# Performance work log

Measured on AMD Instinct MI355X. Metric: run time of the kernel, lower is better.

## Reference

```python
import jax, jax.numpy as jnp
import numpy as np
from jax import lax

B, N, SEG, T = 64, 19, 15, 400
FIN, HID, K, NH, DM, FF, L, NC = 64, 128, 4, 4, 64, 128, 4, 3
EPS = 1e-5


def setup_inputs() -> dict:
    key = jax.random.key(0)
    ks = jax.random.split(key, 40)
    nrm = lambda i, s, sc=0.05: jax.random.normal(ks[i], s, dtype=jnp.float32) * sc
    inp = {
        "X": jax.random.normal(ks[0], (B, N, SEG, T), dtype=jnp.float32),
        "A_hat": jax.random.uniform(ks[1], (B, K, SEG, N, N), dtype=jnp.float32),
        "conv1_w": nrm(2, (32, 1, 25)), "conv1_b": nrm(3, (32,)),
        "conv2_w": nrm(4, (64, 32, 9)), "conv2_b": nrm(5, (64,)),
        "g1_W": nrm(6, (HID, FIN)), "g1_q": nrm(7, (K,), 1.0),
        "g1_bn_g": jnp.ones((HID,)), "g1_bn_b": jnp.zeros((HID,)),
        "g1_bn_m": jnp.zeros((HID,)), "g1_bn_v": jnp.ones((HID,)),
        "g2_W": nrm(8, (FIN, HID)), "g2_q": nrm(9, (K,), 1.0),
        "g2_bn_g": jnp.ones((FIN,)), "g2_bn_b": jnp.zeros((FIN,)),
        "g2_bn_m": jnp.zeros((FIN,)), "g2_bn_v": jnp.ones((FIN,)),
        "cls_token": nrm(10, (1, 1, DM), 0.02), "pos_emb": nrm(11, (1, SEG + 1, DM), 0.02),
        "t_wqkv": nrm(12, (L, 3 * DM, DM)), "t_bqkv": nrm(13, (L, 3 * DM)),
        "t_wo": nrm(14, (L, DM, DM)), "t_bo": nrm(15, (L, DM)),
        "t_ln1g": jnp.ones((L, DM)), "t_ln1b": jnp.zeros((L, DM)),
        "t_w1": nrm(16, (L, FF, DM)), "t_b1": nrm(17, (L, FF)),
        "t_w2": nrm(18, (L, DM, FF)), "t_b2": nrm(19, (L, DM)),
        "t_ln2g": jnp.ones((L, DM)), "t_ln2b": jnp.zeros((L, DM)),
        "clf_w": nrm(20, (NC, DM)), "clf_b": nrm(21, (NC,)),
    }
    return inp


def _ln(x, g, b):
    mu = x.mean(-1, keepdims=True)
    v = ((x - mu) ** 2).mean(-1, keepdims=True)
    return (x - mu) * lax.rsqrt(v + EPS) * g + b


def _maxpool(x, w):  # x: [M, C, T]
    return lax.reduce_window(x, -jnp.inf, lax.max, (1, 1, w), (1, 1, w), "VALID")


def _temporal_encoder(X, c1w, c1b, c2w, c2b):
    # X: [B, SEG, N, T] -> [B, SEG, N, FIN]
    x = X.reshape(-1, 1, T)
    dn = ("NCH", "OIH", "NCH")
    x = lax.conv_general_dilated(x, c1w, (4,), [(12, 12)], dimension_numbers=dn) + c1b[None, :, None]
    x = _maxpool(jax.nn.relu(x), 4)                      # [M,32,25]
    x = lax.conv_general_dilated(x, c2w, (2,), [(4, 4)], dimension_numbers=dn) + c2b[None, :, None]
    x = _maxpool(jax.nn.relu(x), 2)                      # [M,64,6]
    x = x.mean(-1)                                       # AdaptiveAvgPool1d(1)
    return x.reshape(B, SEG, N, FIN)


def _gcn(Xf, A, W, q, g, b, m, v):
    alpha = jax.nn.softmax(q)                            # [K]
    AX = jnp.einsum("bksnm,bsmf->bksnf", A, Xf)          # K-hop diffusion
    Hk = jnp.einsum("bksnf,of->bksno", AX, W)            # shared linear
    H = jnp.einsum("k,bksno->bsno", alpha, Hk)           # attn-weighted hop mix
    H = (H - m) * lax.rsqrt(v + EPS) * g + b             # eval-mode BatchNorm1d
    return jax.nn.relu(H)


def _forward(X, A_hat, conv1_w, conv1_b, conv2_w, conv2_b,
             g1_W, g1_q, g1_bn_g, g1_bn_b, g1_bn_m, g1_bn_v,
             g2_W, g2_q, g2_bn_g, g2_bn_b, g2_bn_m, g2_bn_v,
             cls_token, pos_emb, t_wqkv, t_bqkv, t_wo, t_bo,
             t_ln1g, t_ln1b, t_w1, t_b1, t_w2, t_b2, t_ln2g, t_ln2b,
             clf_w, clf_b):
    Xs = X.reshape(-1, N, SEG, T).transpose(0, 2, 1, 3)  # [B,SEG,N,T]
    feat = _temporal_encoder(Xs, conv1_w, conv1_b, conv2_w, conv2_b)
    H = _gcn(feat, A_hat, g1_W, g1_q, g1_bn_g, g1_bn_b, g1_bn_m, g1_bn_v)
    H = _gcn(H, A_hat, g2_W, g2_q, g2_bn_g, g2_bn_b, g2_bn_m, g2_bn_v)
    g = H.mean(axis=2)                                   # node-mean -> [B,SEG,DM]
    x = jnp.concatenate([jnp.broadcast_to(cls_token, (B, 1, DM)), g], axis=1)
    x = x + pos_emb[:, : SEG + 1]
    dh = DM // NH
    for l in range(L):
        qkv = x @ t_wqkv[l].T + t_bqkv[l]
        qh, kh, vh = [u.reshape(B, SEG + 1, NH, dh).transpose(0, 2, 1, 3)
                      for u in jnp.split(qkv, 3, axis=-1)]
        attn = jax.nn.softmax(jnp.einsum("bhqd,bhkd->bhqk", qh, kh) / jnp.sqrt(jnp.float32(dh)), axis=-1)
        o = jnp.einsum("bhqk,bhkd->bhqd", attn, vh).transpose(0, 2, 1, 3).reshape(B, SEG + 1, DM)
        x = _ln(x + o @ t_wo[l].T + t_bo[l], t_ln1g[l], t_ln1b[l])
        ff = jax.nn.relu(x @ t_w1[l].T + t_b1[l]) @ t_w2[l].T + t_b2[l]
        x = _ln(x + ff, t_ln2g[l], t_ln2b[l])
    return x[:, 0] @ clf_w.T + clf_b                     # [B, NC]


def reference(X, A_hat, conv1_w, conv1_b, conv2_w, conv2_b,
              g1_W, g1_q, g1_bn_g, g1_bn_b, g1_bn_m, g1_bn_v,
              g2_W, g2_q, g2_bn_g, g2_bn_b, g2_bn_m, g2_bn_v,
              cls_token, pos_emb, t_wqkv, t_bqkv, t_wo, t_bo,
              t_ln1g, t_ln1b, t_w1, t_b1, t_w2, t_b2, t_ln2g, t_ln2b,
              clf_w, clf_b):
    return _forward(X, A_hat, conv1_w, conv1_b, conv2_w, conv2_b,
                    g1_W, g1_q, g1_bn_g, g1_bn_b, g1_bn_m, g1_bn_v,
                    g2_W, g2_q, g2_bn_g, g2_bn_b, g2_bn_m, g2_bn_v,
                    cls_token, pos_emb, t_wqkv, t_bqkv, t_wo, t_bo,
                    t_ln1g, t_ln1b, t_w1, t_b1, t_w2, t_b2, t_ln2g, t_ln2b,
                    clf_w, clf_b)
```

## Files before the change

### kernel.cpp

```cpp
#include <hip/hip_runtime.h>
#include <cmath>

#define B_ 64
#define N_ 19
#define SEG_ 15
#define T_ 400
#define FIN_ 64
#define HID_ 128
#define K_ 4
#define NH_ 4
#define DM_ 64
#define FF_ 128
#define L_ 4
#define NC_ 3
#define EPS_ 1e-5f

typedef __attribute__((ext_vector_type(8))) short bf16x8;
typedef __attribute__((ext_vector_type(4))) float f32x4;
typedef unsigned short ushort_t;

__device__ __forceinline__ ushort_t f2bf(float x) {
  union { float f; unsigned u; } a; a.f = x;
  unsigned r = a.u + 0x7fffu + ((a.u >> 16) & 1u);
  return (ushort_t)(r >> 16);
}
__device__ __forceinline__ float bf2f(ushort_t h) {
  union { unsigned u; float f; } a; a.u = ((unsigned)h) << 16;
  return a.f;
}

__global__ __launch_bounds__(256) void k_prep(
    const float* __restrict__ c2w,
    const float* __restrict__ wqkv, const float* __restrict__ wo,
    const float* __restrict__ w1, const float* __restrict__ w2,
    const float* __restrict__ g1W, const float* __restrict__ g2W,
    ushort_t* __restrict__ bt,
    ushort_t* __restrict__ Th, ushort_t* __restrict__ Tl,
    ushort_t* __restrict__ W1h, ushort_t* __restrict__ W1l,
    ushort_t* __restrict__ W2h, ushort_t* __restrict__ W2l) {
  int gid = blockIdx.x * 256 + threadIdx.x;
  if (gid < 18944) {
    int oc = gid / 296, k = gid - oc * 296;
    int ic = k & 31, kk = k >> 5;
    ushort_t v = 0;
    if (kk < 9) v = f2bf(c2w[oc * 288 + ic * 9 + kk]);
    bt[gid] = v;
  } else if (gid < 68096) {
    int i = gid - 18944;
    int l = i / 12288, r = i % 12288;
    float v = wqkv[i];
    ushort_t h = f2bf(v);
    int dst = l * 32768 + r;
    Th[dst] = h; Tl[dst] = f2bf(v - bf2f(h));
  } else if (gid < 84480) {
    int i = gid - 68096;
    int l = i / 4096, r = i % 4096;
    float v = wo[i];
    ushort_t h = f2bf(v);
    int dst = l * 32768 + 12288 + r;
    Th[dst] = h; Tl[dst] = f2bf(v - bf2f(h));
  } else if (gid < 117248) {
    int i = gid - 84480;
    int l = i / 8192, r = i % 8192;
    float v = w1[i];
    ushort_t h = f2bf(v);
    int dst = l * 32768 + 16384 + r;
    Th[dst] = h; Tl[dst] = f2bf(v - bf2f(h));
  } else if (gid < 150016) {
    int i = gid - 117248;
    int l = i / 8192, r = i % 8192;
    float v = w2[i];
    ushort_t h = f2bf(v);
    int dst = l * 32768 + 24576 + r;
    Th[dst] = h; Tl[dst] = f2bf(v - bf2f(h));
  } else if (gid < 158208) {
    int i = gid - 150016;
    float v = g1W[i];
    ushort_t h = f2bf(v);
    W1h[i] = h;
    W1l[i] = f2bf(v - bf2f(h));
  } else if (gid < 166400) {
    int i = gid - 158208;
    float v = g2W[i];
    ushort_t h = f2bf(v);
    W2h[i] = h;
    W2l[i] = f2bf(v - bf2f(h));
  }
}

#define RPB 4
#define ICP 40
#define P1R 40
#define OFFB_XP 0
#define OFFB_W1 6784
#define OFFB_P1 9984
#define SMEM_T 22784

__global__ __launch_bounds__(256, 4) void k_temporal(
    const float* __restrict__ X, const float* __restrict__ c1w,
    const float* __restrict__ c1b, const float* __restrict__ c2b,
    const ushort_t* __restrict__ BmatT, float* __restrict__ Xf) {
  __shared__ __align__(16) unsigned char smem[SMEM_T];
  float* xp  = (float*)(smem + OFFB_XP);
  float* w1s = (float*)(smem + OFFB_W1);
  ushort_t* p1T = (ushort_t*)(smem + OFFB_P1);
  float* Dbuf = (float*)(smem + OFFB_XP);

  const int tid = threadIdx.x;
  const int row0 = blockIdx.x * RPB;

  for (int i = tid; i < 800; i += 256) w1s[i] = c1w[i];
  for (int i = tid; i < RPB * P1R * ICP / 2; i += 256) ((unsigned*)p1T)[i] = 0u;
  for (int r = 0; r < RPB; ++r) {
    const int gr = row0 + r;
    const int n = gr % N_;
    const int s = (gr / N_) % SEG_;
    const int b = gr / (N_ * SEG_);
    const float* xin = X + (((size_t)b * N_ + n) * SEG_ + s) * T_;
    for (int i = tid; i < 424; i += 256) {
      int t = i - 12;
      xp[r * 424 + i] = (t >= 0 && t < T_) ? xin[t] : 0.f;
    }
  }
  __syncthreads();

  {
    const int oc = tid & 31, sub = tid >> 5;
    float wr[25];
#pragma unroll
    for (int k = 0; k < 25; ++k) wr[k] = w1s[oc * 25 + k];
    const float bias = c1b[oc];
    for (int r = 0; r < RPB; ++r) {
      const float* xb = xp + r * 424;
      for (int j = sub; j < 25; j += 8) {
        float xr[37];
#pragma unroll
        for (int k = 0; k < 37; ++k) xr[k] = xb[16 * j + k];
        float m = -1e30f;
#pragma unroll
        for (int p = 0; p < 4; ++p) {
          float acc = bias;
#pragma unroll
          for (int k = 0; k < 25; ++k) acc += xr[4 * p + k] * wr[k];
          m = fmaxf(m, acc);
        }
        p1T[(r * P1R + j + 4) * ICP + oc] = f2bf(fmaxf(m, 0.f));
      }
    }
  }
  __syncthreads();

  const int lane = tid & 63, wv = tid >> 6;
  const int quad = lane >> 4, nl = lane & 15;
  f32x4 acc[4];
  int abase[4];
#pragma unroll
  for (int tm = 0; tm < 4; ++tm) {
    acc[tm] = (f32x4){0.f, 0.f, 0.f, 0.f};
    int m = tm * 16 + nl;
    int rl = m / 14;
    int op = m - rl * 14;
    if (rl > 3) rl = 3;
    if (op > 13) op = 13;
    abase[tm] = (rl * P1R + 2 * op) * ICP + quad * 8;
  }
  const ushort_t* brow = BmatT + (wv * 16 + nl) * 296 + quad * 8;
#pragma unroll
  for (int kk = 0; kk < 9; ++kk) {
    bf16x8 bfr = *(const bf16x8*)(brow + kk * 32);
#pragma unroll
    for (int tm = 0; tm < 4; ++tm) {
      bf16x8 afr = *(const bf16x8*)(p1T + abase[tm] + kk * ICP);
      acc[tm] = __builtin_amdgcn_mfma_f32_16x16x32_bf16(afr, bfr, acc[tm], 0, 0, 0);
    }
  }
  __syncthreads();

#pragma unroll
  for (int tm = 0; tm < 4; ++tm)
#pragma unroll
    for (int rg = 0; rg < 4; ++rg)
      Dbuf[(tm * 16 + quad * 4 + rg) * 66 + wv * 16 + nl] = acc[tm][rg];
  __syncthreads();

  for (int o = tid; o < RPB * 64; o += 256) {
    int rl = o >> 6, oc = o & 63;
    float bias = c2b[oc];
    const float* dr = Dbuf + (rl * 14) * 66 + oc;
    float s = 0.f;
#pragma unroll
    for (int jj = 0; jj < 6; ++jj) {
      float v = fmaxf(dr[(2 * jj) * 66], dr[(2 * jj + 1) * 66]) + bias;
      s += fmaxf(v, 0.f);
    }
    Xf[(size_t)(row0 + rl) * FIN_ + oc] = s * (1.f / 6.f);
  }
}

__global__ __launch_bounds__(256) void k_gcn(
    const float* __restrict__ A, const float* __restrict__ Xf,
    const ushort_t* __restrict__ W1h, const ushort_t* __restrict__ W1l,
    const ushort_t* __restrict__ W2h, const ushort_t* __restrict__ W2l,
    const float* __restrict__ q1, const float* __restrict__ q2,
    const float* __restrict__ b1g, const float* __restrict__ b1b,
    const float* __restrict__ b1m, const float* __restrict__ b1v,
    const float* __restrict__ b2g, const float* __restrict__ b2b,
    const float* __restrict__ b2m, const float* __restrict__ b2v,
    float* __restrict__ G) {
  const int bs = blockIdx.x;
  const int b = bs / SEG_;
  const int s = bs % SEG_;
  const int tid = threadIdx.x;

  __shared__ __align__(16) ushort_t xh[32 * 72], xl[32 * 72];
  __shared__ __align__(16) ushort_t Hh[32 * 136], Hl[32 * 136];
  __shared__ float abar1[N_ * N_], abar2[N_ * N_];
  __shared__ float ybuf[N_ * 130];
  __shared__ float zbuf[N_ * 64];
  __shared__ float sc1[HID_], sh1[HID_], sc2[FIN_], sh2[FIN_];

  {
    float p0 = q1[0], p1 = q1[1], p2 = q1[2], p3 = q1[3];
    float mx = fmaxf(fmaxf(p0, p1), fmaxf(p2, p3));
    float e0 = expf(p0 - mx), e1 = expf(p1 - mx), e2 = expf(p2 - mx), e3 = expf(p3 - mx);
    float inv = 1.f / (e0 + e1 + e2 + e3);
    float a0 = e0 * inv, a1 = e1 * inv, a2 = e2 * inv, a3 = e3 * inv;
    float r0 = q2[0], r1 = q2[1], r2 = q2[2], r3 = q2[3];
    float mx2 = fmaxf(fmaxf(r0, r1), fmaxf(r2, r3));
    float f0 = expf(r0 - mx2), f1 = expf(r1 - mx2), f2 = expf(r2 - mx2), f3 = expf(r3 - mx2);
    float inv2 = 1.f / (f0 + f1 + f2 + f3);
    float c0 = f0 * inv2, c1 = f1 * inv2, c2 = f2 * inv2, c3 = f3 * inv2;
    const size_t kstride = (size_t)SEG_ * N_ * N_;
    const float* Ab = A + ((size_t)b * K_ * SEG_ + s) * (N_ * N_);
    for (int i = tid; i < N_ * N_; i += 256) {
      float v0 = Ab[i], v1 = Ab[i + kstride], v2 = Ab[i + 2 * kstride], v3 = Ab[i + 3 * kstride];
      abar1[i] = a0 * v0 + a1 * v1 + a2 * v2 + a3 * v3;
      abar2[i] = c0 * v0 + c1 * v1 + c2 * v2 + c3 * v3;
    }
  }

  for (int i = tid; i < 32 * 72 / 2; i += 256) {
    ((unsigned*)xh)[i] = 0u; ((unsigned*)xl)[i] = 0u;
  }
  for (int i = tid; i < 32 * 136 / 2; i += 256) {
    ((unsigned*)Hh)[i] = 0u; ((unsigned*)Hl)[i] = 0u;
  }
  for (int o = tid; o < HID_; o += 256) {
    float sc = b1g[o] * rsqrtf(b1v[o] + EPS_);
    sc1[o] = sc; sh1[o] = b1b[o] - b1m[o] * sc;
  }
  for (int o = tid; o < FIN_; o += 256) {
    float sc = b2g[o] * rsqrtf(b2v[o] + EPS_);
    sc2[o] = sc; sh2[o] = b2b[o] - b2m[o] * sc;
  }
  __syncthreads();

  const float* xb = Xf + (size_t)bs * N_ * FIN_;
  for (int i = tid; i < N_ * FIN_; i += 256) {
    int r = i >> 6, f = i & 63;
    float v = xb[i];
    ushort_t h = f2bf(v);
    xh[r * 72 + f] = h;
    xl[r * 72 + f] = f2bf(v - bf2f(h));
  }
  __syncthreads();

  const int lane = tid & 63, wv = tid >> 6;
  const int quad = lane >> 4, nl = lane & 15;

#pragma unroll
  for (int mt = 0; mt < 2; ++mt) {
#pragma unroll
    for (int ntl = 0; ntl < 2; ++ntl) {
      const int nt = wv * 2 + ntl;
      f32x4 acc = (f32x4){0.f, 0.f, 0.f, 0.f};
#pragma unroll
      for (int ks = 0; ks < 2; ++ks) {
        bf16x8 ah = *(const bf16x8*)(xh + (mt * 16 + nl) * 72 + ks * 32 + quad * 8);
        bf16x8 al = *(const bf16x8*)(xl + (mt * 16 + nl) * 72 + ks * 32 + quad * 8);
        bf16x8 bh = *(const bf16x8*)(W1h + (nt * 16 + nl) * 64 + ks * 32 + quad * 8);
        bf16x8 bl = *(const bf16x8*)(W1l + (nt * 16 + nl) * 64 + ks * 32 + quad * 8);
        acc = __builtin_amdgcn_mfma_f32_16x16x32_bf16(ah, bh, acc, 0, 0, 0);
        acc = __builtin_amdgcn_mfma_f32_16x16x32_bf16(al, bh, acc, 0, 0, 0);
        acc = __builtin_amdgcn_mfma_f32_16x16x32_bf16(ah, bl, acc, 0, 0, 0);
      }
#pragma unroll
      for (int r = 0; r < 4; ++r) {
        int m = mt * 16 + quad * 4 + r;
        if (m < N_) ybuf[m * 130 + nt * 16 + nl] = acc[r];
      }
    }
  }
  __syncthreads();

  for (int idx = tid; idx < N_ * HID_; idx += 256) {
    int nn = idx >> 7, o = idx & 127;
    float acc = 0.f;
    const float* ar = &abar1[nn * N_];
#pragma unroll
    for (int m = 0; m < N_; ++m) acc += ar[m] * ybuf[m * 130 + o];
    float h = fmaxf(acc * sc1[o] + sh1[o], 0.f);
    ushort_t hh = f2bf(h);
    Hh[nn * 136 + o] = hh;
    Hl[nn * 136 + o] = f2bf(h - bf2f(hh));
  }
  __syncthreads();

  {
    const int nt = wv;
#pragma unroll
    for (int mt = 0; mt < 2; ++mt) {
      f32x4 acc = (f32x4){0.f, 0.f, 0.f, 0.f};
#pragma unroll
      for (int ks = 0; ks < 4; ++ks) {
        bf16x8 ah = *(const bf16x8*)(Hh + (mt * 16 + nl) * 136 + ks * 32 + quad * 8);
        bf16x8 al = *(const bf16x8*)(Hl + (mt * 16 + nl) * 136 + ks * 32 + quad * 8);
        bf16x8 bh = *(const bf16x8*)(W2h + (nt * 16 + nl) * 128 + ks * 32 + quad * 8);
        bf16x8 bl = *(const bf16x8*)(W2l + (nt * 16 + nl) * 128 + ks * 32 + quad * 8);
        acc = __builtin_amdgcn_mfma_f32_16x16x32_bf16(ah, bh, acc, 0, 0, 0);
        acc = __builtin_amdgcn_mfma_f32_16x16x32_bf16(al, bh, acc, 0, 0, 0);
        acc = __builtin_amdgcn_mfma_f32_16x16x32_bf16(ah, bl, acc, 0, 0, 0);
      }
#pragma unroll
      for (int r = 0; r < 4; ++r) {
        int m = mt * 16 + quad * 4 + r;
        if (m < N_) ybuf[m * 66 + nt * 16 + nl] = acc[r];
      }
    }
  }
  __syncthreads();

  for (int idx = tid; idx < N_ * FIN_; idx += 256) {
    int nn = idx >> 6, o = idx & 63;
    float acc = 0.f;
    const float* ar = &abar2[nn * N_];
#pragma unroll
    for (int m = 0; m < N_; ++m) acc += ar[m] * ybuf[m * 66 + o];
    zbuf[idx] = fmaxf(acc * sc2[o] + sh2[o], 0.f);
  }
  __syncthreads();

  if (tid < FIN_) {
    float ssum = 0.f;
#pragma unroll
    for (int nn = 0; nn < N_; ++nn) ssum += zbuf[nn * 64 + tid];
    G[(size_t)bs * FIN_ + tid] = ssum * (1.f / (float)N_);
  }
}

__global__ __launch_bounds__(256) void k_transformer(
    const float* __restrict__ G, const float* __restrict__ cls,
    const float* __restrict__ pos,
    const ushort_t* __restrict__ Th, const ushort_t* __restrict__ Tl,
    const float* __restrict__ bqkv, const float* __restrict__ bo,
    const float* __restrict__ ln1g, const float* __restrict__ ln1b,
    const float* __restrict__ b1, const float* __restrict__ b2,
    const float* __restrict__ ln2g, const float* __restrict__ ln2b,
    const float* __restrict__ clfw, const float* __restrict__ clfb,
    float* __restrict__ out) {
  const int b = blockIdx.x;
  const int tid = threadIdx.x;
  const int lane = tid & 63, wv = tid >> 6;
  const int quad = lane >> 4, nl = lane & 15;

  __shared__ float xbuf[16 * 64];
  __shared__ __align__(16) ushort_t xh[16 * 72], xl[16 * 72];
  __shared__ float qkvb[16 * 196];
  __shared__ float scb[NH_ * 16 * 16];
  __shared__ __align__(16) ushort_t oh[16 * 72], ol[16 * 72];
  __shared__ __align__(16) ushort_t h1h[16 * 136], h1l[16 * 136];
  __shared__ float tmpb[16 * 64];

  for (int i = tid; i < 16 * 64; i += 256) {
    int t = i >> 6, d = i & 63;
    float base = (t == 0) ? cls[d] : G[((size_t)b * SEG_ + (t - 1)) * DM_ + d];
    float v = base + pos[t * DM_ + d];
    xbuf[i] = v;
    ushort_t h = f2bf(v);
    xh[t * 72 + d] = h;
    xl[t * 72 + d] = f2bf(v - bf2f(h));
  }
  __syncthreads();

  for (int l = 0; l < L_; ++l) {
    const ushort_t* TH = Th + l * 32768;
    const ushort_t* TL = Tl + l * 32768;

#pragma unroll
    for (int ntl = 0; ntl < 3; ++ntl) {
      const int nt = wv * 3 + ntl;
      f32x4 acc = (f32x4){0.f, 0.f, 0.f, 0.f};
#pragma unroll
      for (int ks = 0; ks < 2; ++ks) {
        bf16x8 ah = *(const bf16x8*)(xh + nl * 72 + ks * 32 + quad * 8);
        bf16x8 al = *(const bf16x8*)(xl + nl * 72 + ks * 32 + quad * 8);
        bf16x8 bh = *(const bf16x8*)(TH + (nt * 16 + nl) * 64 + ks * 32 + quad * 8);
        bf16x8 bl = *(const bf16x8*)(TL + (nt * 16 + nl) * 64 + ks * 32 + quad * 8);
        acc = __builtin_amdgcn_mfma_f32_16x16x32_bf16(ah, bh, acc, 0, 0, 0);
        acc = __builtin_amdgcn_mfma_f32_16x16x32_bf16(al, bh, acc, 0, 0, 0);
        acc = __builtin_amdgcn_mfma_f32_16x16x32_bf16(ah, bl, acc, 0, 0, 0);
      }
      const int j = nt * 16 + nl;
      const float bias = bqkv[l * 192 + j];
#pragma unroll
      for (int r = 0; r < 4; ++r)
        qkvb[(quad * 4 + r) * 196 + j] = acc[r] + bias;
    }
    __syncthreads();

    for (int idx = tid; idx < 1024; idx += 256) {
      int h = idx >> 8, t = (idx >> 4) & 15, u = idx & 15;
      const float* qr = &qkvb[t * 196 + h * 16];
      const float* kr = &qkvb[u * 196 + 64 + h * 16];
      float acc = 0.f;
#pragma unroll
      for (int d = 0; d < 16; ++d) acc += qr[d] * kr[d];
      scb[idx] = acc * 0.25f;
    }
    __syncthreads();

    {
      int row = tid >> 2, qq = tid & 3;
      float* r = &scb[row * 16 + qq * 4];
      float v0 = r[0], v1 = r[1], v2 = r[2], v3 = r[3];
      float mxv = fmaxf(fmaxf(v0, v1), fmaxf(v2, v3));
      mxv = fmaxf(mxv, __shfl_xor(mxv, 1));
      mxv = fmaxf(mxv, __shfl_xor(mxv, 2));
      v0 = expf(v0 - mxv); v1 = expf(v1 - mxv);
      v2 = expf(v2 - mxv); v3 = expf(v3 - mxv);
      float sum = v0 + v1 + v2 + v3;
      sum += __shfl_xor(sum, 1);
      sum += __shfl_xor(sum, 2);
      float is = 1.f / sum;
      r[0] = v0 * is; r[1] = v1 * is; r[2] = v2 * is; r[3] = v3 * is;
    }
    __syncthreads();

    for (int idx = tid; idx < 1024; idx += 256) {
      int t = idx >> 6, e = idx & 63, h = e >> 4, d = e & 15;
      const float* pr = &scb[(h * 16 + t) * 16];
      float acc = 0.f;
#pragma unroll
      for (int u = 0; u < 16; ++u) acc += pr[u] * qkvb[u * 196 + 128 + h * 16 + d];
      ushort_t hh = f2bf(acc);
      oh[t * 72 + e] = hh;
      ol[t * 72 + e] = f2bf(acc - bf2f(hh));
    }
    __syncthreads();

    {
      const int nt = wv;
      f32x4 acc = (f32x4){0.f, 0.f, 0.f, 0.f};
#pragma unroll
      for (int ks = 0; ks < 2; ++ks) {
        bf16x8 ah = *(const bf16x8*)(oh + nl * 72 + ks * 32 + quad * 8);
        bf16x8 al = *(const bf16x8*)(ol + nl * 72 + ks * 32 + quad * 8);
        bf16x8 bh = *(const bf16x8*)(TH + 12288 + (nt * 16 + nl) * 64 + ks * 32 + quad * 8);
        bf16x8 bl = *(const bf16x8*)(TL + 12288 + (nt * 16 + nl) * 64 + ks * 32 + quad * 8);
        acc = __builtin_amdgcn_mfma_f32_16x16x32_bf16(ah, bh, acc, 0, 0, 0);
        acc = __builtin_amdgcn_mfma_f32_16x16x32_bf16(al, bh, acc, 0, 0, 0);
        acc = __builtin_amdgcn_mfma_f32_16x16x32_bf16(ah, bl, acc, 0, 0, 0);
      }
      const int d = nt * 16 + nl;
      const float bias = bo[l * 64 + d];
#pragma unroll
      for (int r = 0; r < 4; ++r) {
        int t = quad * 4 + r;
        tmpb[t * 64 + d] = xbuf[t * 64 + d] + acc[r] + bias;
      }
    }
    __syncthreads();

    {
      int t = tid >> 4, i2 = tid & 15;
      float4 v = ((const float4*)(tmpb + t * 64))[i2];
      float s = v.x + v.y + v.z + v.w;
      s += __shfl_xor(s, 1); s += __shfl_xor(s, 2);
      s += __shfl_xor(s, 4); s += __shfl_xor(s, 8);
      float mu = s * (1.f / 64.f);
      float d0 = v.x - mu, d1 = v.y - mu, d2 = v.z - mu, d3 = v.w - mu;
      float vr = d0 * d0 + d1 * d1 + d2 * d2 + d3 * d3;
      vr += __shfl_xor(vr, 1); vr += __shfl_xor(vr, 2);
      vr += __shfl_xor(vr, 4); vr += __shfl_xor(vr, 8);
      float rs = rsqrtf(vr * (1.f / 64.f) + EPS_);
      float4 g4 = ((const float4*)(ln1g + l * 64))[i2];
      float4 b4 = ((const float4*)(ln1b + l * 64))[i2];
      float4 o4;
      o4.x = d0 * rs * g4.x + b4.x; o4.y = d1 * rs * g4.y + b4.y;
      o4.z = d2 * rs * g4.z + b4.z; o4.w = d3 * rs * g4.w + b4.w;
      ((float4*)(xbuf + t * 64))[i2] = o4;
      int base = t * 72 + i2 * 4;
      ushort_t h0 = f2bf(o4.x), h1 = f2bf(o4.y), h2 = f2bf(o4.z), h3 = f2bf(o4.w);
      xh[base + 0] = h0; xh[base + 1] = h1; xh[base + 2] = h2; xh[base + 3] = h3;
      xl[base + 0] = f2bf(o4.x - bf2f(h0));
      xl[base + 1] = f2bf(o4.y - bf2f(h1));
      xl[base + 2] = f2bf(o4.z - bf2f(h2));
      xl[base + 3] = f2bf(o4.w - bf2f(h3));
    }
    __syncthreads();

#pragma unroll
    for (int ntl = 0; ntl < 2; ++ntl) {
      const int nt = wv * 2 + ntl;
      f32x4 acc = (f32x4){0.f, 0.f, 0.f, 0.f};
#pragma unroll
      for (int ks = 0; ks < 2; ++ks) {
        bf16x8 ah = *(const bf16x8*)(xh + nl * 72 + ks * 32 + quad * 8);
        bf16x8 al = *(const bf16x8*)(xl + nl * 72 + ks * 32 + quad * 8);
        bf16x8 bh = *(const bf16x8*)(TH + 16384 + (nt * 16 + nl) * 64 + ks * 32 + quad * 8);
        bf16x8 bl = *(const bf16x8*)(TL + 16384 + (nt * 16 + nl) * 64 + ks * 32 + quad * 8);
        acc = __builtin_amdgcn_mfma_f32_16x16x32_bf16(ah, bh, acc, 0, 0, 0);
        acc = __builtin_amdgcn_mfma_f32_16x16x32_bf16(al, bh, acc, 0, 0, 0);
        acc = __builtin_amdgcn_mfma_f32_16x16x32_bf16(ah, bl, acc, 0, 0, 0);
      }
      const int f = nt * 16 + nl;
      const float bias = b1[l * 128 + f];
#pragma unroll
      for (int r = 0; r < 4; ++r) {
        int t = quad * 4 + r;
        float v = fmaxf(acc[r] + bias, 0.f);
        ushort_t hh = f2bf(v);
        h1h[t * 136 + f] = hh;
        h1l[t * 136 + f] = f2bf(v - bf2f(hh));
      }
    }
    __syncthreads();

    {
      const int nt = wv;
      f32x4 acc = (f32x4){0.f, 0.f, 0.f, 0.f};
#pragma unroll
      for (int ks = 0; ks < 4; ++ks) {
        bf16x8 ah = *(const bf16x8*)(h1h + nl * 136 + ks * 32 + quad * 8);
        bf16x8 al = *(const bf16x8*)(h1l + nl * 136 + ks * 32 + quad * 8);
        bf16x8 bh = *(const bf16x8*)(TH + 24576 + (nt * 16 + nl) * 128 + ks * 32 + quad * 8);
        bf16x8 bl = *(const bf16x8*)(TL + 24576 + (nt * 16 + nl) * 128 + ks * 32 + quad * 8);
        acc = __builtin_amdgcn_mfma_f32_16x16x32_bf16(ah, bh, acc, 0, 0, 0);
        acc = __builtin_amdgcn_mfma_f32_16x16x32_bf16(al, bh, acc, 0, 0, 0);
        acc = __builtin_amdgcn_mfma_f32_16x16x32_bf16(ah, bl, acc, 0, 0, 0);
      }
      const int d = nt * 16 + nl;
      const float bias = b2[l * 64 + d];
#pragma unroll
      for (int r = 0; r < 4; ++r) {
        int t = quad * 4 + r;
        tmpb[t * 64 + d] = xbuf[t * 64 + d] + acc[r] + bias;
      }
    }
    __syncthreads();

    {
      int t = tid >> 4, i2 = tid & 15;
      float4 v = ((const float4*)(tmpb + t * 64))[i2];
      float s = v.x + v.y + v.z + v.w;
      s += __shfl_xor(s, 1); s += __shfl_xor(s, 2);
      s += __shfl_xor(s, 4); s += __shfl_xor(s, 8);
      float mu = s * (1.f / 64.f);
      float d0 = v.x - mu, d1 = v.y - mu, d2 = v.z - mu, d3 = v.w - mu;
      float vr = d0 * d0 + d1 * d1 + d2 * d2 + d3 * d3;
      vr += __shfl_xor(vr, 1); vr += __shfl_xor(vr, 2);
      vr += __shfl_xor(vr, 4); vr += __shfl_xor(vr, 8);
      float rs = rsqrtf(vr * (1.f / 64.f) + EPS_);
      float4 g4 = ((const float4*)(ln2g + l * 64))[i2];
      float4 b4 = ((const float4*)(ln2b + l * 64))[i2];
      float4 o4;
      o4.x = d0 * rs * g4.x + b4.x; o4.y = d1 * rs * g4.y + b4.y;
      o4.z = d2 * rs * g4.z + b4.z; o4.w = d3 * rs * g4.w + b4.w;
      ((float4*)(xbuf + t * 64))[i2] = o4;
      int base = t * 72 + i2 * 4;
      ushort_t h0 = f2bf(o4.x), h1 = f2bf(o4.y), h2 = f2bf(o4.z), h3 = f2bf(o4.w);
      xh[base + 0] = h0; xh[base + 1] = h1; xh[base + 2] = h2; xh[base + 3] = h3;
      xl[base + 0] = f2bf(o4.x - bf2f(h0));
      xl[base + 1] = f2bf(o4.y - bf2f(h1));
      xl[base + 2] = f2bf(o4.z - bf2f(h2));
      xl[base + 3] = f2bf(o4.w - bf2f(h3));
    }
    __syncthreads();
  }

  if (tid < NC_) {
    float acc = clfb[tid];
    const float* wr = &clfw[tid * DM_];
    for (int d = 0; d < DM_; ++d) acc += xbuf[d] * wr[d];
    out[b * NC_ + tid] = acc;
  }
}

extern "C" void kernel_launch(void* const* d_in, const int* in_sizes, int n_in,
                              void* d_out, int out_size, void* d_ws, size_t ws_size,
                              hipStream_t stream) {
  (void)in_sizes; (void)n_in; (void)out_size; (void)ws_size;
  const float* X    = (const float*)d_in[0];
  const float* A    = (const float*)d_in[1];
  const float* c1w  = (const float*)d_in[2];
  const float* c1b  = (const float*)d_in[3];
  const float* c2w  = (const float*)d_in[4];
  const float* c2b  = (const float*)d_in[5];
  const float* g1W  = (const float*)d_in[6];
  const float* g1q  = (const float*)d_in[7];
  const float* g1g  = (const float*)d_in[8];
  const float* g1b  = (const float*)d_in[9];
  const float* g1m  = (const float*)d_in[10];
  const float* g1v  = (const float*)d_in[11];
  const float* g2W  = (const float*)d_in[12];
  const float* g2q  = (const float*)d_in[13];
  const float* g2g  = (const float*)d_in[14];
  const float* g2b  = (const float*)d_in[15];
  const float* g2m  = (const float*)d_in[16];
  const float* g2v  = (const float*)d_in[17];
  const float* cls  = (const float*)d_in[18];
  const float* pos  = (const float*)d_in[19];
  const float* wqkv = (const float*)d_in[20];
  const float* bqkv = (const float*)d_in[21];
  const float* wo   = (const float*)d_in[22];
  const float* bo   = (const float*)d_in[23];
  const float* ln1g = (const float*)d_in[24];
  const float* ln1b = (const float*)d_in[25];
  const float* w1   = (const float*)d_in[26];
  const float* b1   = (const float*)d_in[27];
  const float* w2   = (const float*)d_in[28];
  const float* b2   = (const float*)d_in[29];
  const float* ln2g = (const float*)d_in[30];
  const float* ln2b = (const float*)d_in[31];
  const float* clfw = (const float*)d_in[32];
  const float* clfb = (const float*)d_in[33];
  float* out = (float*)d_out;

  char* wsb = (char*)d_ws;
  ushort_t* BmatT = (ushort_t*)(wsb + 0);
  ushort_t* Th  = (ushort_t*)(wsb + 37888);
  ushort_t* Tl  = (ushort_t*)(wsb + 300032);
  ushort_t* W1h = (ushort_t*)(wsb + 562176);
  ushort_t* W1l = (ushort_t*)(wsb + 578560);
  ushort_t* W2h = (ushort_t*)(wsb + 594944);
  ushort_t* W2l = (ushort_t*)(wsb + 611328);
  float* Xf   = (float*)(wsb + 627712);
  float* G    = (float*)(wsb + 5297152);

  k_prep<<<650, 256, 0, stream>>>(c2w, wqkv, wo, w1, w2, g1W, g2W,
                                  BmatT, Th, Tl, W1h, W1l, W2h, W2l);
  k_temporal<<<B_ * SEG_ * N_ / RPB, 256, 0, stream>>>(
      X, c1w, c1b, c2b, BmatT, Xf);
  k_gcn<<<B_ * SEG_, 256, 0, stream>>>(A, Xf, W1h, W1l, W2h, W2l,
                                       g1q, g2q, g1g, g1b, g1m, g1v,
                                       g2g, g2b, g2m, g2v, G);
  k_transformer<<<B_, 256, 0, stream>>>(G, cls, pos, Th, Tl,
                                        bqkv, bo, ln1g, ln1b, b1, b2, ln2g, ln2b,
                                        clfw, clfb, out);
}
```

Baseline: 253.4 us.

## Move conv1 to split-bf16 MFMA and fuse attention softmax into one pass

The first temporal convolution now runs on MFMA instead of scalar FMA loops. The input is staged as hi/lo bf16 pairs in shared memory, conv1 weights are pre-split into padded hi/lo bf16 in the prep kernel, and the max-pool is taken over the MFMA accumulator rows. In the transformer, the scores, softmax and PV steps are merged into one per-head wave pass with shuffles, which removes two block barriers and the separate score stage. The split-bf16 trick aims to keep near-fp32 accuracy at the cost of three MFMAs per tile plus extra prep and workspace.

```diff
diff --git a/kernel.cpp b/kernel.cpp
--- a/kernel.cpp
+++ b/kernel.cpp
@@ -16,6 +16,7 @@
 #define EPS_ 1e-5f
 
 typedef __attribute__((ext_vector_type(8))) short bf16x8;
+typedef __attribute__((ext_vector_type(4))) short bf16x4;
 typedef __attribute__((ext_vector_type(4))) float f32x4;
 typedef unsigned short ushort_t;
 
@@ -30,14 +31,15 @@
 }
 
 __global__ __launch_bounds__(256) void k_prep(
-    const float* __restrict__ c2w,
+    const float* __restrict__ c1w, const float* __restrict__ c2w,
     const float* __restrict__ wqkv, const float* __restrict__ wo,
     const float* __restrict__ w1, const float* __restrict__ w2,
     const float* __restrict__ g1W, const float* __restrict__ g2W,
     ushort_t* __restrict__ bt,
     ushort_t* __restrict__ Th, ushort_t* __restrict__ Tl,
     ushort_t* __restrict__ W1h, ushort_t* __restrict__ W1l,
-    ushort_t* __restrict__ W2h, ushort_t* __restrict__ W2l) {
+    ushort_t* __restrict__ W2h, ushort_t* __restrict__ W2l,
+    ushort_t* __restrict__ C1h, ushort_t* __restrict__ C1l) {
   int gid = blockIdx.x * 256 + threadIdx.x;
   if (gid < 18944) {
     int oc = gid / 296, k = gid - oc * 296;
@@ -85,73 +87,89 @@
     ushort_t h = f2bf(v);
     W2h[i] = h;
     W2l[i] = f2bf(v - bf2f(h));
+  } else if (gid < 167424) {
+    int i = gid - 166400;
+    int oc = i >> 5, kk = i & 31;
+    float v = (kk < 25) ? c1w[oc * 25 + kk] : 0.f;
+    ushort_t h = f2bf(v);
+    C1h[i] = h;
+    C1l[i] = f2bf(v - bf2f(h));
   }
 }
 
 #define RPB 4
 #define ICP 40
 #define P1R 40
-#define OFFB_XP 0
-#define OFFB_W1 6784
-#define OFFB_P1 9984
-#define SMEM_T 22784
+#define OFF_XPH 0
+#define OFF_XPL 3840
+#define OFF_P1  7680
+#define SMEM_T  20480
 
 __global__ __launch_bounds__(256, 4) void k_temporal(
-    const float* __restrict__ X, const float* __restrict__ c1w,
-    const float* __restrict__ c1b, const float* __restrict__ c2b,
+    const float* __restrict__ X, const float* __restrict__ c1b,
+    const float* __restrict__ c2b,
+    const ushort_t* __restrict__ C1h, const ushort_t* __restrict__ C1l,
     const ushort_t* __restrict__ BmatT, float* __restrict__ Xf) {
   __shared__ __align__(16) unsigned char smem[SMEM_T];
-  float* xp  = (float*)(smem + OFFB_XP);
-  float* w1s = (float*)(smem + OFFB_W1);
-  ushort_t* p1T = (ushort_t*)(smem + OFFB_P1);
-  float* Dbuf = (float*)(smem + OFFB_XP);
+  ushort_t* xph = (ushort_t*)(smem + OFF_XPH);
+  ushort_t* xpl = (ushort_t*)(smem + OFF_XPL);
+  ushort_t* p1T = (ushort_t*)(smem + OFF_P1);
+  float* Dbuf = (float*)smem;
 
   const int tid = threadIdx.x;
   const int row0 = blockIdx.x * RPB;
-
-  for (int i = tid; i < 800; i += 256) w1s[i] = c1w[i];
-  for (int i = tid; i < RPB * P1R * ICP / 2; i += 256) ((unsigned*)p1T)[i] = 0u;
+  const int lane = tid & 63, wv = tid >> 6;
+  const int quad = lane >> 4, nl = lane & 15;
+
+  for (int i = tid; i < 3200; i += 256) ((unsigned*)p1T)[i] = 0u;
   for (int r = 0; r < RPB; ++r) {
     const int gr = row0 + r;
     const int n = gr % N_;
     const int s = (gr / N_) % SEG_;
     const int b = gr / (N_ * SEG_);
-    const float* xin = X + (((size_t)b * N_ + n) * SEG_ + s) * T_;
-    for (int i = tid; i < 424; i += 256) {
-      int t = i - 12;
-      xp[r * 424 + i] = (t >= 0 && t < T_) ? xin[t] : 0.f;
+    const float* xin = X + (((size_t)b * N_ + n) * SEG_ + s) * T_ - 12;
+    for (int i = tid; i < 480; i += 256) {
+      float v = (i >= 12 && i < 412) ? xin[i] : 0.f;
+      ushort_t h = f2bf(v);
+      xph[r * 480 + i] = h;
+      xpl[r * 480 + i] = f2bf(v - bf2f(h));
     }
   }
   __syncthreads();
 
   {
-    const int oc = tid & 31, sub = tid >> 5;
-    float wr[25];
-#pragma unroll
-    for (int k = 0; k < 25; ++k) wr[k] = w1s[oc * 25 + k];
-    const float bias = c1b[oc];
-    for (int r = 0; r < RPB; ++r) {
-      const float* xb = xp + r * 424;
-      for (int j = sub; j < 25; j += 8) {
-        float xr[37];
-#pragma unroll
-        for (int k = 0; k < 37; ++k) xr[k] = xb[16 * j + k];
-        float m = -1e30f;
-#pragma unroll
-        for (int p = 0; p < 4; ++p) {
-          float acc = bias;
-#pragma unroll
-          for (int k = 0; k < 25; ++k) acc += xr[4 * p + k] * wr[k];
-          m = fmaxf(m, acc);
-        }
-        p1T[(r * P1R + j + 4) * ICP + oc] = f2bf(fmaxf(m, 0.f));
-      }
-    }
-  }
-  __syncthreads();
-
-  const int lane = tid & 63, wv = tid >> 6;
-  const int quad = lane >> 4, nl = lane & 15;
+    bf16x8 bh0 = *(const bf16x8*)(C1h + nl * 32 + quad * 8);
+    bf16x8 bh1 = *(const bf16x8*)(C1h + (16 + nl) * 32 + quad * 8);
+    bf16x8 bl0 = *(const bf16x8*)(C1l + nl * 32 + quad * 8);
+    bf16x8 bl1 = *(const bf16x8*)(C1l + (16 + nl) * 32 + quad * 8);
+    const float bias0 = c1b[nl], bias1 = c1b[16 + nl];
+    for (int t = wv; t < 28; t += 4) {
+      const int r = t / 7, mt = t - r * 7;
+      const int aoff = r * 480 + mt * 64 + nl * 4 + quad * 8;
+      union { bf16x4 q[2]; bf16x8 v; } ah, al;
+      ah.q[0] = *(const bf16x4*)(xph + aoff);
+      ah.q[1] = *(const bf16x4*)(xph + aoff + 4);
+      al.q[0] = *(const bf16x4*)(xpl + aoff);
+      al.q[1] = *(const bf16x4*)(xpl + aoff + 4);
+      f32x4 a0 = (f32x4){0.f, 0.f, 0.f, 0.f};
+      a0 = __builtin_amdgcn_mfma_f32_16x16x32_bf16(ah.v, bh0, a0, 0, 0, 0);
+      a0 = __builtin_amdgcn_mfma_f32_16x16x32_bf16(al.v, bh0, a0, 0, 0, 0);
+      a0 = __builtin_amdgcn_mfma_f32_16x16x32_bf16(ah.v, bl0, a0, 0, 0, 0);
+      f32x4 a1 = (f32x4){0.f, 0.f, 0.f, 0.f};
+      a1 = __builtin_amdgcn_mfma_f32_16x16x32_bf16(ah.v, bh1, a1, 0, 0, 0);
+      a1 = __builtin_amdgcn_mfma_f32_16x16x32_bf16(al.v, bh1, a1, 0, 0, 0);
+      a1 = __builtin_amdgcn_mfma_f32_16x16x32_bf16(ah.v, bl1, a1, 0, 0, 0);
+      const int j = mt * 4 + quad;
+      if (j < 25) {
+        float m0 = fmaxf(fmaxf(a0[0], a0[1]), fmaxf(a0[2], a0[3]));
+        float m1 = fmaxf(fmaxf(a1[0], a1[1]), fmaxf(a1[2], a1[3]));
+        p1T[(r * P1R + j + 4) * ICP + nl] = f2bf(fmaxf(m0 + bias0, 0.f));
+        p1T[(r * P1R + j + 4) * ICP + 16 + nl] = f2bf(fmaxf(m1 + bias1, 0.f));
+      }
+    }
+  }
+  __syncthreads();
+
   f32x4 acc[4];
   int abase[4];
 #pragma unroll
@@ -366,7 +384,7 @@
   __shared__ float xbuf[16 * 64];
   __shared__ __align__(16) ushort_t xh[16 * 72], xl[16 * 72];
   __shared__ float qkvb[16 * 196];
-  __shared__ float scb[NH_ * 16 * 16];
+  __shared__ float scb[NH_ * 272];
   __shared__ __align__(16) ushort_t oh[16 * 72], ol[16 * 72];
   __shared__ __align__(16) ushort_t h1h[16 * 136], h1l[16 * 136];
   __shared__ float tmpb[16 * 64];
@@ -408,43 +426,45 @@
     }
     __syncthreads();
 
-    for (int idx = tid; idx < 1024; idx += 256) {
-      int h = idx >> 8, t = (idx >> 4) & 15, u = idx & 15;
-      const float* qr = &qkvb[t * 196 + h * 16];
-      const float* kr = &qkvb[u * 196 + 64 + h * 16];
-      float acc = 0.f;
-#pragma unroll
-      for (int d = 0; d < 16; ++d) acc += qr[d] * kr[d];
-      scb[idx] = acc * 0.25f;
-    }
-    __syncthreads();
-
     {
-      int row = tid >> 2, qq = tid & 3;
-      float* r = &scb[row * 16 + qq * 4];
-      float v0 = r[0], v1 = r[1], v2 = r[2], v3 = r[3];
-      float mxv = fmaxf(fmaxf(v0, v1), fmaxf(v2, v3));
-      mxv = fmaxf(mxv, __shfl_xor(mxv, 1));
-      mxv = fmaxf(mxv, __shfl_xor(mxv, 2));
-      v0 = expf(v0 - mxv); v1 = expf(v1 - mxv);
-      v2 = expf(v2 - mxv); v3 = expf(v3 - mxv);
-      float sum = v0 + v1 + v2 + v3;
-      sum += __shfl_xor(sum, 1);
-      sum += __shfl_xor(sum, 2);
-      float is = 1.f / sum;
-      r[0] = v0 * is; r[1] = v1 * is; r[2] = v2 * is; r[3] = v3 * is;
-    }
-    __syncthreads();
-
-    for (int idx = tid; idx < 1024; idx += 256) {
-      int t = idx >> 6, e = idx & 63, h = e >> 4, d = e & 15;
-      const float* pr = &scb[(h * 16 + t) * 16];
-      float acc = 0.f;
-#pragma unroll
-      for (int u = 0; u < 16; ++u) acc += pr[u] * qkvb[u * 196 + 128 + h * 16 + d];
-      ushort_t hh = f2bf(acc);
-      oh[t * 72 + e] = hh;
-      ol[t * 72 + e] = f2bf(acc - bf2f(hh));
+      const int h = wv;
+      float sc[4];
+      const float* qr = &qkvb[nl * 196 + h * 16];
+#pragma unroll
+      for (int uu = 0; uu < 4; ++uu) {
+        const float* kr = &qkvb[(quad * 4 + uu) * 196 + 64 + h * 16];
+        float a = 0.f;
+#pragma unroll
+        for (int d = 0; d < 16; ++d) a += qr[d] * kr[d];
+        sc[uu] = a * 0.25f;
+      }
+      float mx = fmaxf(fmaxf(sc[0], sc[1]), fmaxf(sc[2], sc[3]));
+      mx = fmaxf(mx, __shfl_xor(mx, 16));
+      mx = fmaxf(mx, __shfl_xor(mx, 32));
+      float e[4];
+      float sum = 0.f;
+#pragma unroll
+      for (int uu = 0; uu < 4; ++uu) { e[uu] = expf(sc[uu] - mx); sum += e[uu]; }
+      sum += __shfl_xor(sum, 16);
+      sum += __shfl_xor(sum, 32);
+      const float is = 1.f / sum;
+      float* prow = &scb[h * 272 + nl * 17];
+#pragma unroll
+      for (int uu = 0; uu < 4; ++uu) prow[quad * 4 + uu] = e[uu] * is;
+      float o[4] = {0.f, 0.f, 0.f, 0.f};
+      for (int u = 0; u < 16; ++u) {
+        float p = prow[u];
+        const float* vr = &qkvb[u * 196 + 128 + h * 16 + quad * 4];
+#pragma unroll
+        for (int dd = 0; dd < 4; ++dd) o[dd] += p * vr[dd];
+      }
+      const int eb = h * 16 + quad * 4;
+#pragma unroll
+      for (int dd = 0; dd < 4; ++dd) {
+        ushort_t hh = f2bf(o[dd]);
+        oh[nl * 72 + eb + dd] = hh;
+        ol[nl * 72 + eb + dd] = f2bf(o[dd] - bf2f(hh));
+      }
     }
     __syncthreads();
 
@@ -634,13 +654,15 @@
   ushort_t* W1l = (ushort_t*)(wsb + 578560);
   ushort_t* W2h = (ushort_t*)(wsb + 594944);
   ushort_t* W2l = (ushort_t*)(wsb + 611328);
-  float* Xf   = (float*)(wsb + 627712);
-  float* G    = (float*)(wsb + 5297152);
-
-  k_prep<<<650, 256, 0, stream>>>(c2w, wqkv, wo, w1, w2, g1W, g2W,
-                                  BmatT, Th, Tl, W1h, W1l, W2h, W2l);
+  ushort_t* C1h = (ushort_t*)(wsb + 627712);
+  ushort_t* C1l = (ushort_t*)(wsb + 629760);
+  float* Xf   = (float*)(wsb + 631808);
+  float* G    = (float*)(wsb + 5301248);
+
+  k_prep<<<654, 256, 0, stream>>>(c1w, c2w, wqkv, wo, w1, w2, g1W, g2W,
+                                  BmatT, Th, Tl, W1h, W1l, W2h, W2l, C1h, C1l);
   k_temporal<<<B_ * SEG_ * N_ / RPB, 256, 0, stream>>>(
-      X, c1w, c1b, c2b, BmatT, Xf);
+      X, c1b, c2b, C1h, C1l, BmatT, Xf);
   k_gcn<<<B_ * SEG_, 256, 0, stream>>>(A, Xf, W1h, W1l, W2h, W2l,
                                        g1q, g2q, g1g, g1b, g1m, g1v,
                                        g2g, g2b, g2m, g2v, G);
```

Result: faster. 224.0 us (-11.6%).
